# Optimization experiments

Hardware: AMD Instinct MI355X
Metric: run time of the kernel (lower is better)

## Reference

```python
import jax, jax.numpy as jnp
import numpy as np

M_ANCH = 704   # 22 parts * 32 anchors
N_ANCH = 128   # object anchors


def reference(smpl_betas, object_rel_rotmat, object_rel_trans, object_anchors_org,
              v_template, shapedirs, J_regressor, pca_mean, pca_components,
              anchor_indices):
    b = smpl_betas.shape[0]
    v = v_template[None] + jnp.einsum('bk,vck->bvc', smpl_betas, shapedirs)   # [b,V,3]
    J = jnp.einsum('jv,bvc->bjc', J_regressor, v)                              # [b,55,3]
    v = v - J[:, :1]                                                           # root-center
    smpl_anchors = v[:, anchor_indices]                                        # [b,704,3]
    # --- encode: transform object anchors, broadcast offset diff, PCA ---
    obj_anchors = jnp.einsum('bnc,bdc->bnd', object_anchors_org, object_rel_rotmat) \
        + object_rel_trans[:, None, :]                                         # [b,128,3]
    offsets = obj_anchors[:, None, :, :] - smpl_anchors[:, :, None, :]         # [b,704,128,3]
    off_flat = offsets.reshape(b, -1)                                          # [b,270336]
    gamma = (off_flat - pca_mean[None]) @ pca_components.T                     # [b,128]
    # --- decode: PCA inverse ---
    off_rec = pca_mean[None] + gamma @ pca_components                          # [b,270336]
    # --- decode_object_RT: batched Procrustes via 3x3 SVD ---
    off4 = off_rec.reshape(b, M_ANCH, N_ANCH, 3)
    P = (smpl_anchors[:, :, None, :] + off4).reshape(b, -1, 3)                 # [b,m*n,3]
    Q = jnp.broadcast_to(object_anchors_org[:, None], (b, M_ANCH, N_ANCH, 3)).reshape(b, -1, 3)
    center_Q = Q.mean(axis=1, keepdims=True)
    Qc = Q - center_Q
    svd_mat = jnp.einsum('bic,bid->bcd', P, Qc)                                # P^T @ Qc, [b,3,3]
    u, s, vh = jnp.linalg.svd(svd_mat, full_matrices=False)
    d = jnp.linalg.det(u @ vh)                                                 # [b]
    dvec = jnp.concatenate([jnp.ones((b, 2), svd_mat.dtype), d[:, None]], axis=-1)
    R = (u * dvec[:, None, :]) @ vh                                            # u @ diag(1,1,d) @ vh
    T = (P - jnp.einsum('bij,bnj->bni', R, Q)).mean(axis=1)                    # [b,3]
    return gamma, R, T


def setup_inputs() -> dict:
    key = jax.random.key(0)
    ks = jax.random.split(key, 10)
    b, V, Jn, K = 64, 10475, 55, 10
    D = M_ANCH * N_ANCH * 3
    return {
        'smpl_betas': jax.random.normal(ks[0], (b, K), jnp.float32),
        'object_rel_rotmat': jax.random.normal(ks[1], (b, 3, 3), jnp.float32),
        'object_rel_trans': jax.random.normal(ks[2], (b, 3), jnp.float32),
        'object_anchors_org': jax.random.normal(ks[3], (b, N_ANCH, 3), jnp.float32),
        'v_template': jax.random.normal(ks[4], (V, 3), jnp.float32),
        'shapedirs': jax.random.normal(ks[5], (V, 3, K), jnp.float32) * 0.03,
        'J_regressor': jax.random.uniform(ks[6], (Jn, V), jnp.float32) / V,
        'pca_mean': jax.random.normal(ks[7], (D,), jnp.float32) * 0.1,
        'pca_components': jax.random.normal(ks[8], (128, D), jnp.float32) / np.sqrt(D),
        'anchor_indices': jax.random.randint(ks[9], (M_ANCH,), 0, V, jnp.int32),
    }
```

## Files before the change

### kernel.cpp

```cpp
#include <hip/hip_runtime.h>

#define V_CNT   10475
#define M_A     704
#define N_A     128
#define KB      10
#define D_TOT   270336
#define ROW384  384
#define NCHUNK  44
#define MT      16
#define LSTR    388

#define WS_JJP    0
#define WS_JJ     960
#define WS_MCP    1024
#define WS_MC     34816
#define WS_CMP    35200
#define WS_CMEAN  40832
#define WS_V2C    40960
#define WS_SAP    41344
#define WS_GWS    42112
#define WS_X      50304
#define WS_WP     210048
#define WS_UPART  529536
#define WS_TOTAL  2692224

#define NJ_BLK 28
#define NM_BLK 88
#define NP_BLK 256

__global__ __launch_bounds__(384) void k_pre(
    const float* __restrict__ Jr, const float* __restrict__ vt,
    const float* __restrict__ sd, const float* __restrict__ mean,
    const float* __restrict__ betas, const float* __restrict__ rot,
    const float* __restrict__ trans, const float* __restrict__ org,
    const int* __restrict__ anch,
    float* __restrict__ JJpart, float* __restrict__ Mcpart,
    float* __restrict__ X, float* __restrict__ sapart) {
  __shared__ float orgL[384];
  __shared__ float red[384];
  __shared__ float small[24];
  __shared__ float jjs[33];
  const int blk = blockIdx.x, t = threadIdx.x;

  if (blk < NJ_BLK) {
    if (t < 33) jjs[t] = 0.f;
    __syncthreads();
    float acc[33];
#pragma unroll
    for (int i = 0; i < 33; ++i) acc[i] = 0.f;
    int v = blk * 384 + t;
    if (v < V_CNT) {
      float jr = Jr[v];
#pragma unroll
      for (int c = 0; c < 3; ++c) {
        acc[c] += jr * vt[v * 3 + c];
        const float* sp = sd + ((size_t)v * 3 + c) * KB;
#pragma unroll
        for (int k = 0; k < KB; ++k) acc[3 + c * KB + k] += jr * sp[k];
      }
    }
#pragma unroll
    for (int i = 0; i < 33; ++i) {
      float x = acc[i];
      for (int off = 32; off > 0; off >>= 1) x += __shfl_down(x, off);
      if ((t & 63) == 0) atomicAdd(&jjs[i], x);
    }
    __syncthreads();
    if (t < 33) JJpart[blk * 33 + t] = jjs[t];
  } else if (blk < NJ_BLK + NM_BLK) {
    int j = blk - NJ_BLK;
    float a = 0.f;
#pragma unroll
    for (int mi = 0; mi < 8; ++mi)
      a += mean[(size_t)(j * 8 + mi) * ROW384 + t];
    Mcpart[(size_t)j * 384 + t] = a;
  } else {
    const int idx = blk - (NJ_BLK + NM_BLK);
    const int b = idx >> 2, sl = idx & 3;
    if (t < 10) small[t] = betas[b * 10 + t];
    else if (t >= 10 && t < 19) small[t] = rot[b * 9 + (t - 10)];
    else if (t >= 19 && t < 22) small[t] = trans[b * 3 + (t - 19)];
    if (sl == 0) orgL[t] = org[(size_t)b * 384 + t];
    __syncthreads();
    if (sl == 0) {
      int n = t / 3, d = t % 3;
      X[(size_t)b * 2496 + t] =
          orgL[n * 3 + 0] * small[10 + d * 3 + 0] +
          orgL[n * 3 + 1] * small[10 + d * 3 + 1] +
          orgL[n * 3 + 2] * small[10 + d * 3 + 2] + small[19 + d];
    }
    float ps = 0.f;
#pragma unroll
    for (int r = 0; r < 2; ++r) {
      int el = t + r * 384;
      if (el < 528) {
        int e = sl * 528 + el;
        int m = e / 3, c = e - m * 3;
        int a = anch[m];
        const float* sp = sd + ((size_t)a * 3 + c) * KB;
        float val = vt[a * 3 + c];
#pragma unroll
        for (int k = 0; k < KB; ++k) val += small[k] * sp[k];
        X[(size_t)b * 2496 + 384 + e] = val;
        ps += val;
      }
    }
    red[t] = ps;
    __syncthreads();
    if (t < 3) {
      float s = 0.f;
#pragma unroll 8
      for (int j = 0; j < 128; ++j) s += red[t + 3 * j];
      sapart[idx * 3 + t] = s;
    }
  }
}

__global__ __launch_bounds__(384) void k_pcpass(
    const float* __restrict__ pc, const float* __restrict__ mean,
    float* __restrict__ Upart, float* __restrict__ Wp,
    float* __restrict__ cmpart) {
  __shared__ float tile[MT * LSTR];
  __shared__ float red[384];
  __shared__ float cred[6];
  const int t = threadIdx.x;
  const int pid = blockIdx.x & 127;
  const int chunk = blockIdx.x >> 7;
  const int m0 = chunk * MT;
  const float* row = pc + (size_t)pid * D_TOT + (size_t)m0 * ROW384;
  const float* mrow = mean + (size_t)m0 * ROW384;

  float cm = 0.f;
#pragma unroll
  for (int i = 0; i < 4; ++i) {
    int f = 1536 * i + 4 * t;
    float4 pv = *(const float4*)(row + f);
    float4 mv = *(const float4*)(mrow + f);
    cm += pv.x * mv.x + pv.y * mv.y + pv.z * mv.z + pv.w * mv.w;
    int m_l = 4 * i + t / 96;
    int col = (t % 96) * 4;
    *(float4*)(&tile[m_l * LSTR + col]) = pv;
  }
  __syncthreads();

  {
    float u = 0.f;
#pragma unroll
    for (int m = 0; m < MT; ++m) u += tile[m * LSTR + t];
    Upart[((size_t)chunk * 128 + pid) * 384 + t] = u;
  }
  {
    int grp = t / 48, mc = t % 48, m_l = mc / 3, c = mc % 3;
    const float* tp = &tile[m_l * LSTR + c];
    float vsp = 0.f;
#pragma unroll 8
    for (int j = 0; j < 16; ++j) vsp += tp[(grp * 16 + j) * 3];
    red[t] = vsp;
  }
  {
    float x = cm;
    for (int off = 32; off > 0; off >>= 1) x += __shfl_down(x, off);
    if ((t & 63) == 0) cred[t >> 6] = x;
  }
  __syncthreads();
  if (t < 48) {
    float vs = 0.f;
#pragma unroll
    for (int g = 0; g < 8; ++g) vs += red[g * 48 + t];
    Wp[(size_t)pid * 2496 + 384 + m0 * 3 + t] = -vs;
  }
  if (t == 0)
    cmpart[chunk * 128 + pid] =
        cred[0] + cred[1] + cred[2] + cred[3] + cred[4] + cred[5];
}

__global__ __launch_bounds__(384) void k_red(
    const float* __restrict__ Upart, const float* __restrict__ JJpart,
    const float* __restrict__ Mcpart, const float* __restrict__ cmpart,
    float* __restrict__ Wp, float* __restrict__ V2c,
    float* __restrict__ JJ, float* __restrict__ Mc,
    float* __restrict__ cmean) {
  const int t = threadIdx.x;
  if (blockIdx.x == 128) {
    if (t < 33) {
      float s = 0.f;
#pragma unroll 4
      for (int j = 0; j < NJ_BLK; ++j) s += JJpart[j * 33 + t];
      JJ[t] = s;
    }
    return;
  }
  if (blockIdx.x == 129) {
    float s = 0.f;
#pragma unroll 4
    for (int j = 0; j < NM_BLK; ++j) s += Mcpart[(size_t)j * 384 + t];
    Mc[t] = s;
    return;
  }
  __shared__ float red[384];
  const int pid = blockIdx.x;
  float u = 0.f;
#pragma unroll 4
  for (int c = 0; c < NCHUNK; ++c)
    u += Upart[((size_t)c * 128 + pid) * 384 + t];
  Wp[(size_t)pid * 2496 + t] = u;
  float s = 0.f;
  const float* vr = Wp + (size_t)pid * 2496 + 384;
#pragma unroll
  for (int j = 0; j < 6; ++j) {
    int idx = t + 384 * j;
    if (idx < 2112) s += vr[idx];
  }
  red[t] = s;
  if (t < 64) {
    float x = (t < NCHUNK) ? cmpart[t * 128 + pid] : 0.f;
#pragma unroll
    for (int off = 32; off > 0; off >>= 1) x += __shfl_down(x, off);
    if (t == 0) cmean[pid] = x;
  }
  __syncthreads();
  if (t < 3) {
    float acc = 0.f;
#pragma unroll 8
    for (int j = 0; j < 128; ++j) acc += red[t + 3 * j];
    V2c[t * 128 + pid] = -acc;
  }
}

__global__ __launch_bounds__(256) void k_gamma(
    const float* __restrict__ X, const float* __restrict__ Wp,
    float* __restrict__ gWS) {
  const int t = threadIdx.x;
  const int b = blockIdx.x >> 5, pg = blockIdx.x & 31;
  const int w = t >> 6, l = t & 63;
  const int p = pg * 4 + w;
  const float4* X4 = (const float4*)(X + (size_t)b * 2496);
  const float4* W4 = (const float4*)(Wp + (size_t)p * 2496);
  float s = 0.f;
#pragma unroll
  for (int i = 0; i < 10; ++i) {
    int idx = i * 64 + l;
    if (idx < 624) {
      float4 xv = X4[idx];
      float4 wv = W4[idx];
      s += xv.x * wv.x + xv.y * wv.y + xv.z * wv.z + xv.w * wv.w;
    }
  }
#pragma unroll
  for (int off = 32; off > 0; off >>= 1) s += __shfl_down(s, off);
  if (l == 0) gWS[b * 128 + p] = s;
}

__device__ inline double det3(const double A[3][3]) {
  return A[0][0] * (A[1][1] * A[2][2] - A[1][2] * A[2][1])
       - A[0][1] * (A[1][0] * A[2][2] - A[1][2] * A[2][0])
       + A[0][2] * (A[1][0] * A[2][1] - A[1][1] * A[2][0]);
}

__device__ void svd3_rotation(const float* S, float* Rout) {
  double M[3][3], B[3][3], Vv[3][3];
  for (int i = 0; i < 3; ++i)
    for (int j = 0; j < 3; ++j) M[i][j] = (double)S[i * 3 + j];
  for (int i = 0; i < 3; ++i)
    for (int j = 0; j < 3; ++j) {
      double a = 0;
      for (int k = 0; k < 3; ++k) a += M[k][i] * M[k][j];
      B[i][j] = a;
    }
  for (int i = 0; i < 3; ++i)
    for (int j = 0; j < 3; ++j) Vv[i][j] = (i == j) ? 1.0 : 0.0;
  const int PP[3] = {0, 0, 1}, QQ[3] = {1, 2, 2};
  for (int sweep = 0; sweep < 25; ++sweep) {
    double off = B[0][1] * B[0][1] + B[0][2] * B[0][2] + B[1][2] * B[1][2];
    double dg = B[0][0] * B[0][0] + B[1][1] * B[1][1] + B[2][2] * B[2][2];
    if (off <= 1e-28 * (dg + 1e-300)) break;
    for (int pr = 0; pr < 3; ++pr) {
      int p = PP[pr], q = QQ[pr];
      double apq = B[p][q];
      if (apq == 0.0) continue;
      double dd = (B[p][p] - B[q][q]) / (2.0 * apq);
      double tt = 1.0 / (fabs(dd) + sqrt(dd * dd + 1.0));
      if (dd < 0.0) tt = -tt;
      double cc = 1.0 / sqrt(tt * tt + 1.0), ss = tt * cc;
      B[p][p] += tt * apq;
      B[q][q] -= tt * apq;
      B[p][q] = B[q][p] = 0.0;
      int k = 3 - p - q;
      double Bkp = cc * B[k][p] + ss * B[k][q];
      double Bkq = -ss * B[k][p] + cc * B[k][q];
      B[k][p] = B[p][k] = Bkp;
      B[k][q] = B[q][k] = Bkq;
      for (int i = 0; i < 3; ++i) {
        double vip = cc * Vv[i][p] + ss * Vv[i][q];
        double viq = -ss * Vv[i][p] + cc * Vv[i][q];
        Vv[i][p] = vip;
        Vv[i][q] = viq;
      }
    }
  }
  double lam[3] = {B[0][0], B[1][1], B[2][2]};
  int o0 = 0, o1 = 1, o2 = 2, tp;
  if (lam[o0] < lam[o1]) { tp = o0; o0 = o1; o1 = tp; }
  if (lam[o0] < lam[o2]) { tp = o0; o0 = o2; o2 = tp; }
  if (lam[o1] < lam[o2]) { tp = o1; o1 = o2; o2 = tp; }
  int ord[3] = {o0, o1, o2};
  double sv[3], U[3][3], Vs[3][3];
  for (int j = 0; j < 3; ++j) {
    double l = lam[ord[j]];
    sv[j] = l > 0.0 ? sqrt(l) : 0.0;
    for (int i = 0; i < 3; ++i) Vs[i][j] = Vv[i][ord[j]];
  }
  for (int j = 0; j < 3; ++j) {
    double vx = Vs[0][j], vy = Vs[1][j], vz = Vs[2][j];
    double ux = M[0][0] * vx + M[0][1] * vy + M[0][2] * vz;
    double uy = M[1][0] * vx + M[1][1] * vy + M[1][2] * vz;
    double uz = M[2][0] * vx + M[2][1] * vy + M[2][2] * vz;
    double sj = sv[j];
    if (sj > 1e-12 * (sv[0] + 1e-300)) {
      U[0][j] = ux / sj; U[1][j] = uy / sj; U[2][j] = uz / sj;
    } else if (j == 2) {
      double cx = U[1][0] * U[2][1] - U[2][0] * U[1][1];
      double cy = U[2][0] * U[0][1] - U[0][0] * U[2][1];
      double cz = U[0][0] * U[1][1] - U[1][0] * U[0][1];
      double nn = sqrt(cx * cx + cy * cy + cz * cz);
      if (nn < 1e-300) { cx = 0; cy = 0; cz = 1; nn = 1; }
      U[0][2] = cx / nn; U[1][2] = cy / nn; U[2][2] = cz / nn;
    } else {
      U[0][j] = (j == 0) ? 1.0 : 0.0;
      U[1][j] = (j == 1) ? 1.0 : 0.0;
      U[2][j] = 0.0;
    }
  }
  double dsgn = (det3(U) * det3(Vs)) < 0.0 ? -1.0 : 1.0;
  for (int i = 0; i < 3; ++i)
    for (int j = 0; j < 3; ++j)
      Rout[i * 3 + j] = (float)(U[i][0] * Vs[j][0] + U[i][1] * Vs[j][1] +
                                dsgn * U[i][2] * Vs[j][2]);
}

__global__ __launch_bounds__(384) void k_finish(
    const float* __restrict__ betas, const float* __restrict__ org,
    const float* __restrict__ JJ, const float* __restrict__ cmean,
    const float* __restrict__ Mc, const float* __restrict__ V2c,
    const float* __restrict__ sapart, const float* __restrict__ gWS,
    const float* __restrict__ Wp, float* __restrict__ out) {
  const int b = blockIdx.x, t = threadIdx.x;
  __shared__ float orgL[384];
  __shared__ __align__(16) float A[384];
  __shared__ float gammaL[128];
  __shared__ float betasL[10], J0L[3], cQ[3], smat[9], RL[9];

  if (t < 10) betasL[t] = betas[b * 10 + t];
  orgL[t] = org[(size_t)b * 384 + t];
  __syncthreads();
  if (t < 3) {
    float j0 = JJ[t];
#pragma unroll
    for (int k = 0; k < KB; ++k) j0 += betasL[k] * JJ[3 + t * KB + k];
    J0L[t] = j0;
    float s = 0.f;
    for (int n = 0; n < N_A; ++n) s += orgL[n * 3 + t];
    cQ[t] = s * (1.f / 128.f);
  }
  __syncthreads();

  if (t < 128) {
    float g = gWS[b * 128 + t] + J0L[0] * V2c[t] + J0L[1] * V2c[128 + t] +
              J0L[2] * V2c[256 + t] - cmean[t];
    gammaL[t] = g;
    out[b * 128 + t] = g;
  }
  __syncthreads();

  if (t < 96) {
    float4 gs = {0.f, 0.f, 0.f, 0.f};
#pragma unroll 4
    for (int p = 0; p < 128; ++p) {
      float4 w = *(const float4*)(Wp + (size_t)p * 2496 + 4 * t);
      float g = gammaL[p];
      gs.x += g * w.x; gs.y += g * w.y; gs.z += g * w.z; gs.w += g * w.w;
    }
    float4 m4 = *(const float4*)(Mc + 4 * t);
    float4 a4 = {m4.x + gs.x, m4.y + gs.y, m4.z + gs.z, m4.w + gs.w};
    *(float4*)(&A[4 * t]) = a4;
  }
  __syncthreads();

  if (t < 9) {
    int c = t / 3, d = t % 3;
    float s = 0.f, cq = cQ[d];
    for (int n = 0; n < N_A; ++n) s += A[n * 3 + c] * (orgL[n * 3 + d] - cq);
    smat[t] = s;
  }
  __syncthreads();
  if (t == 0) svd3_rotation(smat, RL);
  __syncthreads();
  if (t < 9) out[8192 + b * 9 + t] = RL[t];
  if (t < 3) {
    float sSum = sapart[(b * 4 + 0) * 3 + t] + sapart[(b * 4 + 1) * 3 + t] +
                 sapart[(b * 4 + 2) * 3 + t] + sapart[(b * 4 + 3) * 3 + t];
    float s2 = 0.f;
    for (int n = 0; n < N_A; ++n) s2 += A[n * 3 + t];
    float meanP = sSum * (1.f / 704.f) - J0L[t] + s2 * (1.f / 90112.f);
    float rq = RL[t * 3 + 0] * cQ[0] + RL[t * 3 + 1] * cQ[1] + RL[t * 3 + 2] * cQ[2];
    out[8768 + b * 3 + t] = meanP - rq;
  }
}

extern "C" void kernel_launch(void* const* d_in, const int* in_sizes, int n_in,
                              void* d_out, int out_size, void* d_ws, size_t ws_size,
                              hipStream_t stream) {
  const float* betas = (const float*)d_in[0];
  const float* rot   = (const float*)d_in[1];
  const float* trans = (const float*)d_in[2];
  const float* org   = (const float*)d_in[3];
  const float* vt    = (const float*)d_in[4];
  const float* sd    = (const float*)d_in[5];
  const float* Jr    = (const float*)d_in[6];
  const float* mean  = (const float*)d_in[7];
  const float* pc    = (const float*)d_in[8];
  const int*   anch  = (const int*)d_in[9];
  float* out = (float*)d_out;
  float* ws  = (float*)d_ws;
  if (ws_size < (size_t)WS_TOTAL * sizeof(float)) return;

  float* JJpart = ws + WS_JJP;
  float* JJ     = ws + WS_JJ;
  float* Mcpart = ws + WS_MCP;
  float* Mc     = ws + WS_MC;
  float* cmpart = ws + WS_CMP;
  float* cmean  = ws + WS_CMEAN;
  float* V2c    = ws + WS_V2C;
  float* sapart = ws + WS_SAP;
  float* gWS    = ws + WS_GWS;
  float* X      = ws + WS_X;
  float* Wp     = ws + WS_WP;
  float* Upart  = ws + WS_UPART;

  k_pre<<<NJ_BLK + NM_BLK + NP_BLK, 384, 0, stream>>>(
      Jr, vt, sd, mean, betas, rot, trans, org, anch, JJpart, Mcpart, X, sapart);
  k_pcpass<<<NCHUNK * 128, 384, 0, stream>>>(pc, mean, Upart, Wp, cmpart);
  k_red<<<130, 384, 0, stream>>>(Upart, JJpart, Mcpart, cmpart, Wp, V2c, JJ, Mc,
                                 cmean);
  k_gamma<<<64 * 32, 256, 0, stream>>>(X, Wp, gWS);
  k_finish<<<64, 384, 0, stream>>>(betas, org, JJ, cmean, Mc, V2c, sapart, gWS,
                                   Wp, out);
}
```

Before: 265.5 us.

## Fuse pre and PCA pass kernels, fold gamma into reduction, split finish reduction

Merges k_pre and k_pcpass into one launch, and the gamma dot products and bias terms into the per-component reduction kernel, which keeps each Wp row in shared memory. This cuts the launch count from five to three and drops the cmean/V2c round trips. k_finish now splits the gamma·W accumulation across four thread groups instead of 96 threads, and the JJ accumulation is rewritten with a non-unrolled loop to reduce register pressure. The trade-off is that k_red2 runs only 129 blocks, each looping over 64 batches serially, which could lengthen the critical path.

```diff
diff --git a/kernel.cpp b/kernel.cpp
--- a/kernel.cpp
+++ b/kernel.cpp
@@ -15,8 +15,6 @@
 #define WS_MCP    1024
 #define WS_MC     34816
 #define WS_CMP    35200
-#define WS_CMEAN  40832
-#define WS_V2C    40960
 #define WS_SAP    41344
 #define WS_GWS    42112
 #define WS_X      50304
@@ -27,67 +25,120 @@
 #define NJ_BLK 28
 #define NM_BLK 88
 #define NP_BLK 256
-
-__global__ __launch_bounds__(384) void k_pre(
+#define NPC    (NCHUNK * 128)
+
+__global__ __launch_bounds__(384) void k_main(
+    const float* __restrict__ pc, const float* __restrict__ mean,
     const float* __restrict__ Jr, const float* __restrict__ vt,
-    const float* __restrict__ sd, const float* __restrict__ mean,
-    const float* __restrict__ betas, const float* __restrict__ rot,
-    const float* __restrict__ trans, const float* __restrict__ org,
-    const int* __restrict__ anch,
-    float* __restrict__ JJpart, float* __restrict__ Mcpart,
-    float* __restrict__ X, float* __restrict__ sapart) {
-  __shared__ float orgL[384];
+    const float* __restrict__ sd, const float* __restrict__ betas,
+    const float* __restrict__ rot, const float* __restrict__ trans,
+    const float* __restrict__ org, const int* __restrict__ anch,
+    float* __restrict__ Upart, float* __restrict__ Wp,
+    float* __restrict__ cmpart, float* __restrict__ JJpart,
+    float* __restrict__ Mcpart, float* __restrict__ X,
+    float* __restrict__ sapart) {
+  __shared__ float tile[MT * LSTR];
   __shared__ float red[384];
-  __shared__ float small[24];
+  __shared__ float cred[6];
   __shared__ float jjs[33];
   const int blk = blockIdx.x, t = threadIdx.x;
 
-  if (blk < NJ_BLK) {
+  if (blk < NPC) {
+    const int pid = blk & 127;
+    const int chunk = blk >> 7;
+    const int m0 = chunk * MT;
+    const float* row = pc + (size_t)pid * D_TOT + (size_t)m0 * ROW384;
+    const float* mrow = mean + (size_t)m0 * ROW384;
+
+    float cm = 0.f;
+#pragma unroll
+    for (int i = 0; i < 4; ++i) {
+      int f = 1536 * i + 4 * t;
+      float4 pv = *(const float4*)(row + f);
+      float4 mv = *(const float4*)(mrow + f);
+      cm += pv.x * mv.x + pv.y * mv.y + pv.z * mv.z + pv.w * mv.w;
+      int m_l = 4 * i + t / 96;
+      int col = (t % 96) * 4;
+      *(float4*)(&tile[m_l * LSTR + col]) = pv;
+    }
+    __syncthreads();
+
+    {
+      float u = 0.f;
+#pragma unroll
+      for (int m = 0; m < MT; ++m) u += tile[m * LSTR + t];
+      Upart[((size_t)chunk * 128 + pid) * 384 + t] = u;
+    }
+    {
+      int grp = t / 48, mc = t % 48, m_l = mc / 3, c = mc % 3;
+      const float* tp = &tile[m_l * LSTR + c];
+      float vsp = 0.f;
+#pragma unroll 8
+      for (int j = 0; j < 16; ++j) vsp += tp[(grp * 16 + j) * 3];
+      red[t] = vsp;
+    }
+    {
+      float x = cm;
+      for (int off = 32; off > 0; off >>= 1) x += __shfl_down(x, off);
+      if ((t & 63) == 0) cred[t >> 6] = x;
+    }
+    __syncthreads();
+    if (t < 48) {
+      float vs = 0.f;
+#pragma unroll
+      for (int g = 0; g < 8; ++g) vs += red[g * 48 + t];
+      Wp[(size_t)pid * 2496 + 384 + m0 * 3 + t] = -vs;
+    }
+    if (t == 0)
+      cmpart[chunk * 128 + pid] =
+          cred[0] + cred[1] + cred[2] + cred[3] + cred[4] + cred[5];
+    return;
+  }
+
+  const int pblk = blk - NPC;
+  float* orgL = tile;
+  float* smallv = tile + 384;
+
+  if (pblk < NJ_BLK) {
     if (t < 33) jjs[t] = 0.f;
     __syncthreads();
-    float acc[33];
-#pragma unroll
-    for (int i = 0; i < 33; ++i) acc[i] = 0.f;
-    int v = blk * 384 + t;
-    if (v < V_CNT) {
-      float jr = Jr[v];
-#pragma unroll
-      for (int c = 0; c < 3; ++c) {
-        acc[c] += jr * vt[v * 3 + c];
-        const float* sp = sd + ((size_t)v * 3 + c) * KB;
-#pragma unroll
-        for (int k = 0; k < KB; ++k) acc[3 + c * KB + k] += jr * sp[k];
-      }
-    }
-#pragma unroll
+    const int v = pblk * 384 + t;
+    const bool ok = v < V_CNT;
+    const float jr = ok ? Jr[v] : 0.f;
+    const float* vp = vt + (size_t)v * 3;
+    const float* sp = sd + (size_t)v * 30;
+#pragma unroll 1
     for (int i = 0; i < 33; ++i) {
-      float x = acc[i];
-      for (int off = 32; off > 0; off >>= 1) x += __shfl_down(x, off);
-      if ((t & 63) == 0) atomicAdd(&jjs[i], x);
-    }
-    __syncthreads();
-    if (t < 33) JJpart[blk * 33 + t] = jjs[t];
-  } else if (blk < NJ_BLK + NM_BLK) {
-    int j = blk - NJ_BLK;
+      float x = 0.f;
+      if (ok) x = (i < 3) ? vp[i] : sp[i - 3];
+      float val = jr * x;
+#pragma unroll
+      for (int off = 32; off > 0; off >>= 1) val += __shfl_down(val, off);
+      if ((t & 63) == 0) atomicAdd(&jjs[i], val);
+    }
+    __syncthreads();
+    if (t < 33) JJpart[pblk * 33 + t] = jjs[t];
+  } else if (pblk < NJ_BLK + NM_BLK) {
+    int j = pblk - NJ_BLK;
     float a = 0.f;
 #pragma unroll
     for (int mi = 0; mi < 8; ++mi)
       a += mean[(size_t)(j * 8 + mi) * ROW384 + t];
     Mcpart[(size_t)j * 384 + t] = a;
   } else {
-    const int idx = blk - (NJ_BLK + NM_BLK);
+    const int idx = pblk - (NJ_BLK + NM_BLK);
     const int b = idx >> 2, sl = idx & 3;
-    if (t < 10) small[t] = betas[b * 10 + t];
-    else if (t >= 10 && t < 19) small[t] = rot[b * 9 + (t - 10)];
-    else if (t >= 19 && t < 22) small[t] = trans[b * 3 + (t - 19)];
+    if (t < 10) smallv[t] = betas[b * 10 + t];
+    else if (t < 19) smallv[t] = rot[b * 9 + (t - 10)];
+    else if (t < 22) smallv[t] = trans[b * 3 + (t - 19)];
     if (sl == 0) orgL[t] = org[(size_t)b * 384 + t];
     __syncthreads();
     if (sl == 0) {
       int n = t / 3, d = t % 3;
       X[(size_t)b * 2496 + t] =
-          orgL[n * 3 + 0] * small[10 + d * 3 + 0] +
-          orgL[n * 3 + 1] * small[10 + d * 3 + 1] +
-          orgL[n * 3 + 2] * small[10 + d * 3 + 2] + small[19 + d];
+          orgL[n * 3 + 0] * smallv[10 + d * 3 + 0] +
+          orgL[n * 3 + 1] * smallv[10 + d * 3 + 1] +
+          orgL[n * 3 + 2] * smallv[10 + d * 3 + 2] + smallv[19 + d];
     }
     float ps = 0.f;
 #pragma unroll
@@ -100,7 +151,7 @@
         const float* sp = sd + ((size_t)a * 3 + c) * KB;
         float val = vt[a * 3 + c];
 #pragma unroll
-        for (int k = 0; k < KB; ++k) val += small[k] * sp[k];
+        for (int k = 0; k < KB; ++k) val += smallv[k] * sp[k];
         X[(size_t)b * 2496 + 384 + e] = val;
         ps += val;
       }
@@ -116,70 +167,12 @@
   }
 }
 
-__global__ __launch_bounds__(384) void k_pcpass(
-    const float* __restrict__ pc, const float* __restrict__ mean,
-    float* __restrict__ Upart, float* __restrict__ Wp,
-    float* __restrict__ cmpart) {
-  __shared__ float tile[MT * LSTR];
-  __shared__ float red[384];
-  __shared__ float cred[6];
-  const int t = threadIdx.x;
-  const int pid = blockIdx.x & 127;
-  const int chunk = blockIdx.x >> 7;
-  const int m0 = chunk * MT;
-  const float* row = pc + (size_t)pid * D_TOT + (size_t)m0 * ROW384;
-  const float* mrow = mean + (size_t)m0 * ROW384;
-
-  float cm = 0.f;
-#pragma unroll
-  for (int i = 0; i < 4; ++i) {
-    int f = 1536 * i + 4 * t;
-    float4 pv = *(const float4*)(row + f);
-    float4 mv = *(const float4*)(mrow + f);
-    cm += pv.x * mv.x + pv.y * mv.y + pv.z * mv.z + pv.w * mv.w;
-    int m_l = 4 * i + t / 96;
-    int col = (t % 96) * 4;
-    *(float4*)(&tile[m_l * LSTR + col]) = pv;
-  }
-  __syncthreads();
-
-  {
-    float u = 0.f;
-#pragma unroll
-    for (int m = 0; m < MT; ++m) u += tile[m * LSTR + t];
-    Upart[((size_t)chunk * 128 + pid) * 384 + t] = u;
-  }
-  {
-    int grp = t / 48, mc = t % 48, m_l = mc / 3, c = mc % 3;
-    const float* tp = &tile[m_l * LSTR + c];
-    float vsp = 0.f;
-#pragma unroll 8
-    for (int j = 0; j < 16; ++j) vsp += tp[(grp * 16 + j) * 3];
-    red[t] = vsp;
-  }
-  {
-    float x = cm;
-    for (int off = 32; off > 0; off >>= 1) x += __shfl_down(x, off);
-    if ((t & 63) == 0) cred[t >> 6] = x;
-  }
-  __syncthreads();
-  if (t < 48) {
-    float vs = 0.f;
-#pragma unroll
-    for (int g = 0; g < 8; ++g) vs += red[g * 48 + t];
-    Wp[(size_t)pid * 2496 + 384 + m0 * 3 + t] = -vs;
-  }
-  if (t == 0)
-    cmpart[chunk * 128 + pid] =
-        cred[0] + cred[1] + cred[2] + cred[3] + cred[4] + cred[5];
-}
-
-__global__ __launch_bounds__(384) void k_red(
+__global__ __launch_bounds__(384) void k_red2(
     const float* __restrict__ Upart, const float* __restrict__ JJpart,
     const float* __restrict__ Mcpart, const float* __restrict__ cmpart,
-    float* __restrict__ Wp, float* __restrict__ V2c,
-    float* __restrict__ JJ, float* __restrict__ Mc,
-    float* __restrict__ cmean) {
+    const float* __restrict__ betas, const float* __restrict__ X,
+    float* __restrict__ Wp, float* __restrict__ JJ, float* __restrict__ Mc,
+    float* __restrict__ gWS, float* __restrict__ out) {
   const int t = threadIdx.x;
   if (blockIdx.x == 128) {
     if (t < 33) {
@@ -188,67 +181,92 @@
       for (int j = 0; j < NJ_BLK; ++j) s += JJpart[j * 33 + t];
       JJ[t] = s;
     }
-    return;
-  }
-  if (blockIdx.x == 129) {
     float s = 0.f;
 #pragma unroll 4
     for (int j = 0; j < NM_BLK; ++j) s += Mcpart[(size_t)j * 384 + t];
     Mc[t] = s;
     return;
   }
+  __shared__ __align__(16) float Wl[2496];
   __shared__ float red[384];
+  __shared__ float J0s[192];
+  __shared__ float jjl[33];
+  __shared__ float cmv[4];
   const int pid = blockIdx.x;
-  float u = 0.f;
+
+  {
+    float u = 0.f;
 #pragma unroll 4
-  for (int c = 0; c < NCHUNK; ++c)
-    u += Upart[((size_t)c * 128 + pid) * 384 + t];
-  Wp[(size_t)pid * 2496 + t] = u;
-  float s = 0.f;
-  const float* vr = Wp + (size_t)pid * 2496 + 384;
-#pragma unroll
-  for (int j = 0; j < 6; ++j) {
-    int idx = t + 384 * j;
-    if (idx < 2112) s += vr[idx];
-  }
-  red[t] = s;
+    for (int c = 0; c < NCHUNK; ++c)
+      u += Upart[((size_t)c * 128 + pid) * 384 + t];
+    Wp[(size_t)pid * 2496 + t] = u;
+    Wl[t] = u;
+  }
+  {
+    float s = 0.f;
+    const float* vr = Wp + (size_t)pid * 2496 + 384;
+#pragma unroll
+    for (int j = 0; j < 6; ++j) {
+      int idx = t + 384 * j;
+      if (idx < 2112) {
+        float v = vr[idx];
+        Wl[384 + idx] = v;
+        s += v;
+      }
+    }
+    red[t] = s;
+  }
+  if (t < 33) {
+    float a = 0.f;
+#pragma unroll 4
+    for (int j = 0; j < NJ_BLK; ++j) a += JJpart[j * 33 + t];
+    jjl[t] = a;
+  }
   if (t < 64) {
     float x = (t < NCHUNK) ? cmpart[t * 128 + pid] : 0.f;
 #pragma unroll
     for (int off = 32; off > 0; off >>= 1) x += __shfl_down(x, off);
-    if (t == 0) cmean[pid] = x;
+    if (t == 0) cmv[3] = x;
   }
   __syncthreads();
   if (t < 3) {
     float acc = 0.f;
 #pragma unroll 8
     for (int j = 0; j < 128; ++j) acc += red[t + 3 * j];
-    V2c[t * 128 + pid] = -acc;
-  }
-}
-
-__global__ __launch_bounds__(256) void k_gamma(
-    const float* __restrict__ X, const float* __restrict__ Wp,
-    float* __restrict__ gWS) {
-  const int t = threadIdx.x;
-  const int b = blockIdx.x >> 5, pg = blockIdx.x & 31;
+    cmv[t] = -acc;
+  }
+  if (t < 192) {
+    int b = t / 3, c = t - 3 * (t / 3);
+    float j0 = jjl[c];
+#pragma unroll
+    for (int k = 0; k < KB; ++k) j0 += betas[b * 10 + k] * jjl[3 + c * 10 + k];
+    J0s[t] = j0;
+  }
+  __syncthreads();
+
   const int w = t >> 6, l = t & 63;
-  const int p = pg * 4 + w;
-  const float4* X4 = (const float4*)(X + (size_t)b * 2496);
-  const float4* W4 = (const float4*)(Wp + (size_t)p * 2496);
-  float s = 0.f;
-#pragma unroll
-  for (int i = 0; i < 10; ++i) {
-    int idx = i * 64 + l;
-    if (idx < 624) {
-      float4 xv = X4[idx];
-      float4 wv = W4[idx];
-      s += xv.x * wv.x + xv.y * wv.y + xv.z * wv.z + xv.w * wv.w;
-    }
-  }
-#pragma unroll
-  for (int off = 32; off > 0; off >>= 1) s += __shfl_down(s, off);
-  if (l == 0) gWS[b * 128 + p] = s;
+  const float4* W4 = (const float4*)Wl;
+  for (int b = w; b < 64; b += 6) {
+    const float4* X4 = (const float4*)(X + (size_t)b * 2496);
+    float dot = 0.f;
+#pragma unroll
+    for (int i = 0; i < 10; ++i) {
+      int idx = i * 64 + l;
+      if (idx < 624) {
+        float4 xv = X4[idx];
+        float4 wv = W4[idx];
+        dot += xv.x * wv.x + xv.y * wv.y + xv.z * wv.z + xv.w * wv.w;
+      }
+    }
+#pragma unroll
+    for (int off = 32; off > 0; off >>= 1) dot += __shfl_down(dot, off);
+    if (l == 0) {
+      float g = dot + J0s[b * 3 + 0] * cmv[0] + J0s[b * 3 + 1] * cmv[1] +
+                J0s[b * 3 + 2] * cmv[2] - cmv[3];
+      gWS[b * 128 + pid] = g;
+      out[b * 128 + pid] = g;
+    }
+  }
 }
 
 __device__ inline double det3(const double A[3][3]) {
@@ -340,18 +358,19 @@
 
 __global__ __launch_bounds__(384) void k_finish(
     const float* __restrict__ betas, const float* __restrict__ org,
-    const float* __restrict__ JJ, const float* __restrict__ cmean,
-    const float* __restrict__ Mc, const float* __restrict__ V2c,
+    const float* __restrict__ JJ, const float* __restrict__ Mc,
     const float* __restrict__ sapart, const float* __restrict__ gWS,
     const float* __restrict__ Wp, float* __restrict__ out) {
   const int b = blockIdx.x, t = threadIdx.x;
   __shared__ float orgL[384];
   __shared__ __align__(16) float A[384];
+  __shared__ float4 redA[4][96];
   __shared__ float gammaL[128];
   __shared__ float betasL[10], J0L[3], cQ[3], smat[9], RL[9];
 
   if (t < 10) betasL[t] = betas[b * 10 + t];
   orgL[t] = org[(size_t)b * 384 + t];
+  if (t >= 256) gammaL[t - 256] = gWS[b * 128 + (t - 256)];
   __syncthreads();
   if (t < 3) {
     float j0 = JJ[t];
@@ -362,26 +381,27 @@
     for (int n = 0; n < N_A; ++n) s += orgL[n * 3 + t];
     cQ[t] = s * (1.f / 128.f);
   }
-  __syncthreads();
-
-  if (t < 128) {
-    float g = gWS[b * 128 + t] + J0L[0] * V2c[t] + J0L[1] * V2c[128 + t] +
-              J0L[2] * V2c[256 + t] - cmean[t];
-    gammaL[t] = g;
-    out[b * 128 + t] = g;
-  }
-  __syncthreads();
-
+
+  {
+    int grp = t / 96, tn = t - grp * 96;
+    float4 gs = {0.f, 0.f, 0.f, 0.f};
+#pragma unroll 8
+    for (int i = 0; i < 32; ++i) {
+      int p = grp * 32 + i;
+      float4 wv = *(const float4*)(Wp + (size_t)p * 2496 + 4 * tn);
+      float g = gammaL[p];
+      gs.x += g * wv.x; gs.y += g * wv.y; gs.z += g * wv.z; gs.w += g * wv.w;
+    }
+    redA[grp][tn] = gs;
+  }
+  __syncthreads();
   if (t < 96) {
-    float4 gs = {0.f, 0.f, 0.f, 0.f};
-#pragma unroll 4
-    for (int p = 0; p < 128; ++p) {
-      float4 w = *(const float4*)(Wp + (size_t)p * 2496 + 4 * t);
-      float g = gammaL[p];
-      gs.x += g * w.x; gs.y += g * w.y; gs.z += g * w.z; gs.w += g * w.w;
-    }
+    float4 s0 = redA[0][t], s1 = redA[1][t], s2 = redA[2][t], s3 = redA[3][t];
     float4 m4 = *(const float4*)(Mc + 4 * t);
-    float4 a4 = {m4.x + gs.x, m4.y + gs.y, m4.z + gs.z, m4.w + gs.w};
+    float4 a4 = {m4.x + s0.x + s1.x + s2.x + s3.x,
+                 m4.y + s0.y + s1.y + s2.y + s3.y,
+                 m4.z + s0.z + s1.z + s2.z + s3.z,
+                 m4.w + s0.w + s1.w + s2.w + s3.w};
     *(float4*)(&A[4 * t]) = a4;
   }
   __syncthreads();
@@ -429,20 +449,16 @@
   float* Mcpart = ws + WS_MCP;
   float* Mc     = ws + WS_MC;
   float* cmpart = ws + WS_CMP;
-  float* cmean  = ws + WS_CMEAN;
-  float* V2c    = ws + WS_V2C;
   float* sapart = ws + WS_SAP;
   float* gWS    = ws + WS_GWS;
   float* X      = ws + WS_X;
   float* Wp     = ws + WS_WP;
   float* Upart  = ws + WS_UPART;
 
-  k_pre<<<NJ_BLK + NM_BLK + NP_BLK, 384, 0, stream>>>(
-      Jr, vt, sd, mean, betas, rot, trans, org, anch, JJpart, Mcpart, X, sapart);
-  k_pcpass<<<NCHUNK * 128, 384, 0, stream>>>(pc, mean, Upart, Wp, cmpart);
-  k_red<<<130, 384, 0, stream>>>(Upart, JJpart, Mcpart, cmpart, Wp, V2c, JJ, Mc,
-                                 cmean);
-  k_gamma<<<64 * 32, 256, 0, stream>>>(X, Wp, gWS);
-  k_finish<<<64, 384, 0, stream>>>(betas, org, JJ, cmean, Mc, V2c, sapart, gWS,
-                                   Wp, out);
-}
+  k_main<<<NPC + NJ_BLK + NM_BLK + NP_BLK, 384, 0, stream>>>(
+      pc, mean, Jr, vt, sd, betas, rot, trans, org, anch,
+      Upart, Wp, cmpart, JJpart, Mcpart, X, sapart);
+  k_red2<<<129, 384, 0, stream>>>(Upart, JJpart, Mcpart, cmpart, betas, X,
+                                  Wp, JJ, Mc, gWS, out);
+  k_finish<<<64, 384, 0, stream>>>(betas, org, JJ, Mc, sapart, gWS, Wp, out);
+}
```

Measured after the change: 263.7 us. About the same (-0.6%).
